# Optimization experiments

Measured on AMD Instinct MI355X. Metric: run time of the kernel, lower is better.

Reference implementation:

```python
import jax, jax.numpy as jnp
import numpy as np

B, K, D, E, V, T = 128, 49, 512, 256, 10000, 20


def setup_inputs() -> dict:
    key = jax.random.key(0)
    ks = jax.random.split(key, 20)
    rn = lambda k, shape, s=0.02: jax.random.normal(k, shape, jnp.float32) * s
    lengths = jnp.sort(jax.random.randint(ks[3], (B,), 1, T + 1))[::-1]
    lengths = lengths.at[0].set(T)  # max(lengths) == T, sorted descending
    return {
        "spatial": jax.random.normal(ks[0], (B, K, D), jnp.float32),
        "global_feats": jax.random.normal(ks[1], (B, D), jnp.float32),
        "captions": jax.random.randint(ks[2], (B, T), 0, V),
        "lengths": lengths,
        "emb": rn(ks[4], (V, E), 0.05),
        "W_init_h": rn(ks[5], (D, D)), "b_init_h": jnp.zeros((D,), jnp.float32),
        "W_init_m": rn(ks[6], (D, D)), "b_init_m": jnp.zeros((D,), jnp.float32),
        "W_ih": rn(ks[7], (4 * D, E + D)), "b_ih": jnp.zeros((4 * D,), jnp.float32),
        "W_hh": rn(ks[8], (4 * D, D)), "b_hh": jnp.zeros((4 * D,), jnp.float32),
        "Wv": rn(ks[9], (K, D)), "bv": jnp.zeros((K,), jnp.float32),
        "Wg": rn(ks[10], (K, D)), "bg": jnp.zeros((K,), jnp.float32),
        "wh": rn(ks[11], (1, K)), "bh_att": jnp.zeros((1,), jnp.float32),
        "Wp": rn(ks[12], (V, D)), "bp": jnp.zeros((V,), jnp.float32),
    }


def reference(spatial, global_feats, captions, lengths, emb,
              W_init_h, b_init_h, W_init_m, b_init_m,
              W_ih, b_ih, W_hh, b_hh,
              Wv, bv, Wg, bg, wh, bh_att, Wp, bp):
    # initialize_state
    h0 = global_feats @ W_init_h.T + b_init_h  # [B,D]
    m0 = global_feats @ W_init_m.T + b_init_m
    emb_seq = emb[captions]                     # [B,T,E]
    V_proj = spatial @ Wv.T + bv                # [B,K,K] (attn hidden = k), loop-invariant

    def step(carry, xs):
        h, m = carry
        w, t = xs                               # w: [B,E]
        active = (lengths > t)[:, None]         # masked equivalent of shrinking batch
        x = jnp.concatenate([w, global_feats], axis=1)  # [B,E+D]
        gates = x @ W_ih.T + b_ih + h @ W_hh.T + b_hh   # [B,4D]
        i, f, g, o = jnp.split(gates, 4, axis=1)        # torch LSTMCell gate order
        i, f, o = jax.nn.sigmoid(i), jax.nn.sigmoid(f), jax.nn.sigmoid(o)
        g = jnp.tanh(g)
        m_new = f * m + i * g
        h_new = o * jnp.tanh(m_new)
        h = jnp.where(active, h_new, h)
        m = jnp.where(active, m_new, m)
        # spatial attention: z = w_h^T tanh(W_v V + W_g h)
        z = jnp.tanh(V_proj + (h @ Wg.T + bg)[:, None, :]) @ wh[0] + bh_att[0]  # [B,K]
        alpha = jax.nn.softmax(z, axis=1)
        c = jnp.einsum('bk,bkd->bd', alpha, spatial)
        logit = (c + h) @ Wp.T + bp             # [B,V]
        logit = jnp.where(active, logit, 0.0)
        return (h, m), logit

    xs = (emb_seq.transpose(1, 0, 2), jnp.arange(T))
    (_, _), logits = jax.lax.scan(step, (h0, m0), xs)
    return logits.transpose(1, 0, 2)            # [B,T,V]
```

## Files before the change

kernel.cpp:

```cpp
#include <hip/hip_runtime.h>
#include <hip/hip_bf16.h>
#include <math.h>

typedef __bf16 bf16;
typedef __bf16 v8bf __attribute__((ext_vector_type(8)));
typedef __bf16 v4bfv __attribute__((ext_vector_type(4)));
typedef float  v4f  __attribute__((ext_vector_type(4)));

#define B_   128
#define KK_  49
#define D_   512
#define E_   256
#define V_   10000
#define T_   20
#define NG_  2048
#define XK_  768
#define VPAD 10112
#define NP_  128
#define NBLK 64

#define GLOAD_LDS16(gp, lp) \
    __builtin_amdgcn_global_load_lds((const __attribute__((address_space(1))) void*)(gp), \
                                     (__attribute__((address_space(3))) void*)(lp), 16, 0, 0)

__device__ inline v4bfv cvt4(float4 v) {
    v4bfv o; o[0] = (bf16)v.x; o[1] = (bf16)v.y; o[2] = (bf16)v.z; o[3] = (bf16)v.w;
    return o;
}

__global__ void prep_kernel(
    const float* __restrict__ spatial, const float* __restrict__ gfeat,
    const int* __restrict__ caps, const float* __restrict__ emb,
    const float* __restrict__ W_init_h, const float* __restrict__ b_init_h,
    const float* __restrict__ W_init_m, const float* __restrict__ b_init_m,
    const float* __restrict__ W_ih, const float* __restrict__ b_ih,
    const float* __restrict__ W_hh, const float* __restrict__ b_hh,
    const float* __restrict__ Wv, const float* __restrict__ bv,
    const float* __restrict__ Wg, const float* __restrict__ bg,
    const float* __restrict__ Wp,
    bf16* __restrict__ Wp_b, bf16* __restrict__ Whh_b, bf16* __restrict__ Wih_b,
    bf16* __restrict__ Xin_b, bf16* __restrict__ Sp_b,
    bf16* __restrict__ Wv_b, bf16* __restrict__ Wg_b,
    bf16* __restrict__ Winit2_b, bf16* __restrict__ Gf_b,
    float* __restrict__ bias_comb, float* __restrict__ bias_init,
    float* __restrict__ bv_pad, float* __restrict__ bg_pad,
    int* __restrict__ flags)
{
    const int stride = gridDim.x * blockDim.x;
    const int tid0 = blockIdx.x * blockDim.x + threadIdx.x;
    const float4 z4 = make_float4(0.f, 0.f, 0.f, 0.f);

    for (int i = tid0; i < NBLK * 32; i += stride) flags[i] = 0;

    for (int i4 = tid0; i4 < VPAD * D_ / 4; i4 += stride) {
        int row = i4 >> 7;
        float4 v = (row < V_) ? ((const float4*)Wp)[i4] : z4;
        ((v4bfv*)Wp_b)[i4] = cvt4(v);
    }
    for (int i4 = tid0; i4 < NG_ * D_ / 4; i4 += stride)
        ((v4bfv*)Whh_b)[i4] = cvt4(((const float4*)W_hh)[i4]);
    for (int i4 = tid0; i4 < NG_ * XK_ / 4; i4 += stride)
        ((v4bfv*)Wih_b)[i4] = cvt4(((const float4*)W_ih)[i4]);
    for (int i4 = tid0; i4 < T_ * B_ * XK_ / 4; i4 += stride) {
        int r = i4 / (XK_ / 4), c4 = i4 - r * (XK_ / 4);
        int c = c4 * 4;
        int t = r >> 7, b = r & 127;
        float4 v;
        if (c < E_) v = *(const float4*)&emb[(long)caps[b * T_ + t] * E_ + c];
        else        v = *(const float4*)&gfeat[(long)b * D_ + (c - E_)];
        ((v4bfv*)Xin_b)[i4] = cvt4(v);
    }
    for (int i4 = tid0; i4 < B_ * KK_ * D_ / 4; i4 += stride)
        ((v4bfv*)Sp_b)[i4] = cvt4(((const float4*)spatial)[i4]);
    for (int i4 = tid0; i4 < NP_ * D_ / 4; i4 += stride) {
        int row = i4 >> 7;
        ((v4bfv*)Wv_b)[i4] = cvt4((row < KK_) ? ((const float4*)Wv)[i4] : z4);
        ((v4bfv*)Wg_b)[i4] = cvt4((row < KK_) ? ((const float4*)Wg)[i4] : z4);
    }
    for (int i4 = tid0; i4 < 2 * D_ * D_ / 4; i4 += stride) {
        int row = i4 >> 7;
        float4 v = (row < D_) ? ((const float4*)W_init_h)[i4]
                              : ((const float4*)W_init_m)[i4 - D_ * (D_ / 4)];
        ((v4bfv*)Winit2_b)[i4] = cvt4(v);
    }
    for (int i4 = tid0; i4 < B_ * D_ / 4; i4 += stride)
        ((v4bfv*)Gf_b)[i4] = cvt4(((const float4*)gfeat)[i4]);
    for (int i = tid0; i < NG_; i += stride) bias_comb[i] = b_ih[i] + b_hh[i];
    for (int i = tid0; i < 2 * D_; i += stride)
        bias_init[i] = (i < D_) ? b_init_h[i] : b_init_m[i - D_];
    for (int i = tid0; i < NP_; i += stride) {
        bv_pad[i] = (i < KK_) ? bv[i] : 0.f;
        bg_pad[i] = (i < KK_) ? bg[i] : 0.f;
    }
}

template <int OUTMODE>
__global__ __launch_bounds__(256, 4) void gemm_bt(
    const bf16* __restrict__ A, const bf16* __restrict__ Bm,
    const float* __restrict__ bias, void* __restrict__ Cout, void* __restrict__ Cout2,
    int M, int N, int K, int out_stride, int n_real, const int* __restrict__ lengths)
{
    __shared__ bf16 As[2 * 128 * 32];
    __shared__ bf16 Bs[2 * 128 * 32];
    const int m0 = blockIdx.x * 128, n0 = blockIdx.y * 128;
    const int tid = threadIdx.x;
    const int w = tid >> 6, l = tid & 63;
    const int wm = (w >> 1) * 64, wn = (w & 1) * 64;
    const int lr = l & 15, lq = l >> 4;

    v4f acc[4][4] = {};

    for (int k0 = 0; k0 < K; k0 += 64) {
        __syncthreads();
        #pragma unroll
        for (int c = 0; c < 4; c++) {
            int u = c * 256 + tid;
            int h = u >> 9, v = u & 511;
            int row = v >> 2, kc = (v & 3) * 8;
            int u0 = c * 256 + (tid & ~63);
            GLOAD_LDS16(&A[(long)(m0 + row) * K + k0 + h * 32 + kc], &As[u0 * 8]);
            GLOAD_LDS16(&Bm[(long)(n0 + row) * K + k0 + h * 32 + kc], &Bs[u0 * 8]);
        }
        __syncthreads();
        #pragma unroll
        for (int h = 0; h < 2; h++) {
            v8bf af[4], bfv[4];
            #pragma unroll
            for (int s = 0; s < 4; s++) {
                af[s]  = *(const v8bf*)&As[h * 4096 + (wm + s * 16 + lr) * 32 + lq * 8];
                bfv[s] = *(const v8bf*)&Bs[h * 4096 + (wn + s * 16 + lr) * 32 + lq * 8];
            }
            #pragma unroll
            for (int i = 0; i < 4; i++)
                #pragma unroll
                for (int j = 0; j < 4; j++)
                    acc[i][j] = __builtin_amdgcn_mfma_f32_16x16x32_bf16(af[i], bfv[j], acc[i][j], 0, 0, 0);
        }
    }

    #pragma unroll
    for (int i = 0; i < 4; i++)
        #pragma unroll
        for (int j = 0; j < 4; j++)
            #pragma unroll
            for (int r = 0; r < 4; r++) {
                int m = m0 + wm + i * 16 + lq * 4 + r;
                int n = n0 + wn + j * 16 + lr;
                float v = acc[i][j][r];
                if (OUTMODE == 2) {
                    if (n < n_real) {
                        int t = m % T_, b = m / T_;
                        float o = (t < lengths[b]) ? (v + bias[n]) : 0.f;
                        ((float*)Cout)[(long)m * out_stride + n] = o;
                    }
                } else if (OUTMODE == 3) {
                    if (n < D_) ((bf16*)Cout)[(long)m * D_ + n] = (bf16)(v + bias[n]);
                    else ((float*)Cout2)[(long)m * D_ + n - D_] = v + bias[n];
                } else {
                    ((float*)Cout)[(long)m * out_stride + n] = v + bias[n];
                }
            }
}

__global__ __launch_bounds__(256) void lstm_persist(
    bf16* __restrict__ Hb16, const bf16* __restrict__ Whh_b,
    const float* __restrict__ Xpre, const float* __restrict__ mbuf,
    const int* __restrict__ lengths, int* __restrict__ flags)
{
    const int tid = threadIdx.x;
    const int w = tid >> 6, l = tid & 63;
    const int lr = l & 15, lq = l >> 4;
    const int bt = blockIdx.x & 1, dt = blockIdx.x >> 1;
    const int b0 = bt * 64, d0 = dt * 16;

    __shared__ bf16 Bl[64][520];

    for (int u = tid; u < 64 * 64; u += 256) {
        int row = u >> 6, kc = (u & 63) * 8;
        int g = row >> 4, dd = row & 15;
        *(v8bf*)&Bl[row][kc] = *(const v8bf*)&Whh_b[(long)(g * D_ + d0 + dd) * D_ + kc];
    }

    const int d = d0 + lr;
    float m_st[4], h_st[4];
    float xpf[4][4];
    int lenr[4];
    #pragma unroll
    for (int r = 0; r < 4; r++) {
        int b = b0 + w * 16 + lq * 4 + r;
        lenr[r] = lengths[b];
        m_st[r] = mbuf[(long)b * D_ + d];
        h_st[r] = (float)Hb16[(long)b * D_ + d];
        #pragma unroll
        for (int g = 0; g < 4; g++)
            xpf[r][g] = Xpre[(long)b * NG_ + g * D_ + d];
    }
    __syncthreads();

    for (int t = 0; t < T_; t++) {
        const bf16* Arow = Hb16 + (long)t * B_ * D_ + (long)(b0 + w * 16 + lr) * D_;
        v4f acc[4] = {};
        #pragma unroll
        for (int kk = 0; kk < 16; kk++) {
            v8bf a = *(const v8bf*)&Arow[kk * 32 + lq * 8];
            #pragma unroll
            for (int g = 0; g < 4; g++) {
                v8bf bv = *(const v8bf*)&Bl[g * 16 + lr][kk * 32 + lq * 8];
                acc[g] = __builtin_amdgcn_mfma_f32_16x16x32_bf16(a, bv, acc[g], 0, 0, 0);
            }
        }

        bf16* hn = Hb16 + (long)(t + 1) * B_ * D_;
        #pragma unroll
        for (int r = 0; r < 4; r++) {
            int b = b0 + w * 16 + lq * 4 + r;
            float gi = acc[0][r] + xpf[r][0];
            float gf = acc[1][r] + xpf[r][1];
            float gc = acc[2][r] + xpf[r][2];
            float go = acc[3][r] + xpf[r][3];
            gi = 1.f / (1.f + expf(-gi));
            gf = 1.f / (1.f + expf(-gf));
            gc = tanhf(gc);
            go = 1.f / (1.f + expf(-go));
            float m_new = gf * m_st[r] + gi * gc;
            float h_new = go * tanhf(m_new);
            bool active = t < lenr[r];
            m_st[r] = active ? m_new : m_st[r];
            h_st[r] = active ? h_new : h_st[r];
            hn[(long)b * D_ + d] = (bf16)h_st[r];
        }

        if (t + 1 < T_) {
            __syncthreads();
            if (tid == 0) {
                __threadfence();
                __hip_atomic_store(&flags[blockIdx.x * 32], t + 1,
                                   __ATOMIC_RELAXED, __HIP_MEMORY_SCOPE_AGENT);
            }
            #pragma unroll
            for (int r = 0; r < 4; r++) {
                int b = b0 + w * 16 + lq * 4 + r;
                #pragma unroll
                for (int g = 0; g < 4; g++)
                    xpf[r][g] = Xpre[(long)(t + 1) * B_ * NG_ + (long)b * NG_ + g * D_ + d];
            }
            if (w == 0) {
                int need = t + 1, v = need;
                do {
                    if (l < 32)
                        v = __hip_atomic_load(&flags[(2 * l + bt) * 32],
                                              __ATOMIC_RELAXED, __HIP_MEMORY_SCOPE_AGENT);
                } while (__any(v < need));
                __threadfence();
            }
            __syncthreads();
        }
    }
}

__global__ __launch_bounds__(256) void attn_kernel(
    const bf16* __restrict__ Hb16, const float* __restrict__ g_all,
    const float* __restrict__ Vproj, const float* __restrict__ wh,
    const bf16* __restrict__ Sp_b, bf16* __restrict__ ctx)
{
    const int w = threadIdx.x >> 6, l = threadIdx.x & 63;
    const int b = blockIdx.x / 5, tg = blockIdx.x % 5;
    const int t = tg * 4 + w;
    const int r = t * 128 + b;
    __shared__ float svp[KK_][53];
    __shared__ float sg[4][64], sal[4][64], swh[64];

    for (int p = threadIdx.x; p < KK_ * 64; p += 256) {
        int k = p >> 6, j = p & 63;
        if (j < KK_) svp[k][j] = Vproj[((long)b * KK_ + k) * NP_ + j];
    }
    if (w == 0) swh[l] = (l < KK_) ? wh[l] : 0.f;
    sg[w][l] = (l < KK_) ? g_all[(long)r * NP_ + l] : 0.f;
    __syncthreads();

    float z = -1e30f;
    if (l < KK_) {
        float a = 0.f;
        for (int j = 0; j < KK_; j++)
            a += swh[j] * tanhf(svp[l][j] + sg[w][j]);
        z = a;
    }
    float mx = z;
    #pragma unroll
    for (int o = 32; o > 0; o >>= 1) mx = fmaxf(mx, __shfl_xor(mx, o));
    float e = (l < KK_) ? expf(z - mx) : 0.f;
    float sm = e;
    #pragma unroll
    for (int o = 32; o > 0; o >>= 1) sm += __shfl_xor(sm, o);
    sal[w][l] = e / sm;
    __syncthreads();

    const bf16* hrow = Hb16 + (long)(t + 1) * B_ * D_ + (long)b * D_;
    const bf16* sp = Sp_b + (long)b * KK_ * D_;
    bf16* crow = ctx + (long)(b * T_ + t) * D_;
    v8bf hro = *(const v8bf*)&hrow[l * 8];
    float c[8] = {};
    for (int k = 0; k < KK_; k++) {
        v8bf s8 = *(const v8bf*)&sp[k * D_ + l * 8];
        float al = sal[w][k];
        #pragma unroll
        for (int e2 = 0; e2 < 8; e2++) c[e2] += al * (float)s8[e2];
    }
    v8bf outv;
    #pragma unroll
    for (int e2 = 0; e2 < 8; e2++) outv[e2] = (bf16)(c[e2] + (float)hro[e2]);
    *(v8bf*)&crow[l * 8] = outv;
}

extern "C" void kernel_launch(void* const* d_in, const int* in_sizes, int n_in,
                              void* d_out, int out_size, void* d_ws, size_t ws_size,
                              hipStream_t stream)
{
    const float* spatial  = (const float*)d_in[0];
    const float* gfeat    = (const float*)d_in[1];
    const int*   caps     = (const int*)d_in[2];
    const int*   lengths  = (const int*)d_in[3];
    const float* emb      = (const float*)d_in[4];
    const float* W_init_h = (const float*)d_in[5];
    const float* b_init_h = (const float*)d_in[6];
    const float* W_init_m = (const float*)d_in[7];
    const float* b_init_m = (const float*)d_in[8];
    const float* W_ih     = (const float*)d_in[9];
    const float* b_ih     = (const float*)d_in[10];
    const float* W_hh     = (const float*)d_in[11];
    const float* b_hh     = (const float*)d_in[12];
    const float* Wv       = (const float*)d_in[13];
    const float* bv       = (const float*)d_in[14];
    const float* Wg       = (const float*)d_in[15];
    const float* bg       = (const float*)d_in[16];
    const float* wh       = (const float*)d_in[17];
    const float* bh_att   = (const float*)d_in[18];
    const float* Wp       = (const float*)d_in[19];
    const float* bp       = (const float*)d_in[20];
    float* out = (float*)d_out;
    (void)bh_att;

    char* ws = (char*)d_ws;
    size_t off = 0;
    auto alloc = [&](size_t bytes) -> void* {
        off = (off + 255) & ~(size_t)255;
        void* p = ws + off;
        off += bytes;
        return p;
    };

    bf16* Wp_b    = (bf16*)alloc((size_t)VPAD * D_ * 2);
    bf16* Whh_b   = (bf16*)alloc((size_t)NG_ * D_ * 2);
    bf16* Wih_b   = (bf16*)alloc((size_t)NG_ * XK_ * 2);
    bf16* Xin_b   = (bf16*)alloc((size_t)T_ * B_ * XK_ * 2);
    bf16* Sp_b    = (bf16*)alloc((size_t)B_ * KK_ * D_ * 2);
    bf16* Wv_b    = (bf16*)alloc((size_t)NP_ * D_ * 2);
    bf16* Wg_b    = (bf16*)alloc((size_t)NP_ * D_ * 2);
    bf16* Winit2_b= (bf16*)alloc((size_t)2 * D_ * D_ * 2);
    bf16* Gf_b    = (bf16*)alloc((size_t)B_ * D_ * 2);
    float* bias_comb = (float*)alloc(NG_ * 4);
    float* bias_init = (float*)alloc(2 * D_ * 4);
    float* bv_pad    = (float*)alloc(NP_ * 4);
    float* bg_pad    = (float*)alloc(NP_ * 4);
    bf16* Hb16    = (bf16*)alloc((size_t)(T_ + 1) * B_ * D_ * 2);
    float* mbuf   = (float*)alloc((size_t)B_ * D_ * 4);
    float* Xpre   = (float*)alloc((size_t)T_ * B_ * NG_ * 4);
    float* VprojW = (float*)alloc((size_t)B_ * KK_ * NP_ * 4);
    float* g_allW = (float*)alloc((size_t)T_ * B_ * NP_ * 4);
    bf16* ctx     = (bf16*)alloc((size_t)T_ * B_ * D_ * 2);
    int*  flags   = (int*)alloc((size_t)NBLK * 32 * 4);

    prep_kernel<<<1024, 256, 0, stream>>>(
        spatial, gfeat, caps, emb, W_init_h, b_init_h, W_init_m, b_init_m,
        W_ih, b_ih, W_hh, b_hh, Wv, bv, Wg, bg, Wp,
        Wp_b, Whh_b, Wih_b, Xin_b, Sp_b, Wv_b, Wg_b, Winit2_b, Gf_b,
        bias_comb, bias_init, bv_pad, bg_pad, flags);

    gemm_bt<3><<<dim3(1, 8), 256, 0, stream>>>(Gf_b, Winit2_b, bias_init,
                                               Hb16, mbuf, B_, 2 * D_, D_, 0, 0, nullptr);

    gemm_bt<0><<<dim3((B_ * KK_) / 128, 1), 256, 0, stream>>>(
        Sp_b, Wv_b, bv_pad, VprojW, nullptr, B_ * KK_, NP_, D_, NP_, 0, nullptr);

    gemm_bt<0><<<dim3((T_ * B_) / 128, NG_ / 128), 256, 0, stream>>>(
        Xin_b, Wih_b, bias_comb, Xpre, nullptr, T_ * B_, NG_, XK_, NG_, 0, nullptr);

    lstm_persist<<<NBLK, 256, 0, stream>>>(Hb16, Whh_b, Xpre, mbuf, lengths, flags);

    gemm_bt<0><<<dim3((T_ * B_) / 128, 1), 256, 0, stream>>>(
        Hb16 + (size_t)B_ * D_, Wg_b, bg_pad, g_allW, nullptr, T_ * B_, NP_, D_, NP_, 0, nullptr);

    attn_kernel<<<B_ * 5, 256, 0, stream>>>(Hb16, g_allW, VprojW, wh, Sp_b, ctx);

    gemm_bt<2><<<dim3((T_ * B_) / 128, VPAD / 128), 256, 0, stream>>>(
        ctx, Wp_b, bp, out, nullptr, T_ * B_, VPAD, D_, V_, V_, lengths);
}
```

Before: 475.2 us.

## Confine persistent LSTM blocks to a single XCD with leader election

The persistent LSTM kernel now launches a larger grid. Each block reads its XCD id and takes a slot through an atomic counter. The first XCD to gather 32 blocks wins the leader election and runs the recurrence; all other blocks exit. Each surviving block computes 32 hidden columns instead of 16, the explicit threadfences are dropped, and h is written with nontemporal stores. The aim is to keep per-step flag synchronisation inside one XCD's L2 and halve the number of participating blocks, cutting inter-block barrier latency. The cost is relying on same-XCD coherence without fences, plus the extra launch and election overhead.

```diff
diff --git a/kernel.cpp b/kernel.cpp
--- a/kernel.cpp
+++ b/kernel.cpp
@@ -18,6 +18,12 @@
 #define VPAD 10112
 #define NP_  128
 #define NBLK 64
+#define LGRID 256
+
+#define FLG_CNT    1024
+#define FLG_READY  1040
+#define FLG_LEADER 1056
+#define FLG_DONE   1057
 
 #define GLOAD_LDS16(gp, lp) \
     __builtin_amdgcn_global_load_lds((const __attribute__((address_space(1))) void*)(gp), \
@@ -167,95 +173,140 @@
     const float* __restrict__ Xpre, const float* __restrict__ mbuf,
     const int* __restrict__ lengths, int* __restrict__ flags)
 {
+    __shared__ bf16 Bl[128][520];
+    __shared__ int s_info[2];
     const int tid = threadIdx.x;
+
+    if (tid == 0) {
+        int xcd;
+        asm volatile("s_getreg_b32 %0, hwreg(HW_REG_XCC_ID)" : "=s"(xcd));
+        xcd &= 15;
+        int slot = __hip_atomic_fetch_add(&flags[FLG_CNT + xcd], 1,
+                                          __ATOMIC_RELAXED, __HIP_MEMORY_SCOPE_AGENT);
+        if (slot == 31) {
+            int exp = 0;
+            bool win = __hip_atomic_compare_exchange_strong(
+                &flags[FLG_LEADER], &exp, xcd + 1,
+                __ATOMIC_RELAXED, __ATOMIC_RELAXED, __HIP_MEMORY_SCOPE_AGENT);
+            __hip_atomic_store(&flags[FLG_READY + xcd], win ? 1 : 2,
+                               __ATOMIC_RELAXED, __HIP_MEMORY_SCOPE_AGENT);
+        }
+        int st;
+        if (slot < 32) {
+            int dn;
+            do {
+                st = __hip_atomic_load(&flags[FLG_READY + xcd],
+                                       __ATOMIC_RELAXED, __HIP_MEMORY_SCOPE_AGENT);
+                dn = __hip_atomic_load(&flags[FLG_DONE],
+                                       __ATOMIC_RELAXED, __HIP_MEMORY_SCOPE_AGENT);
+            } while (st == 0 && dn == 0);
+            if (st == 0) st = 2;
+        } else st = 2;
+        s_info[0] = st;
+        s_info[1] = slot;
+    }
+    __syncthreads();
+    if (s_info[0] != 1) return;
+
+    const int slot = s_info[1];
     const int w = tid >> 6, l = tid & 63;
     const int lr = l & 15, lq = l >> 4;
-    const int bt = blockIdx.x & 1, dt = blockIdx.x >> 1;
-    const int b0 = bt * 64, d0 = dt * 16;
-
-    __shared__ bf16 Bl[64][520];
-
-    for (int u = tid; u < 64 * 64; u += 256) {
+    const int rh = slot & 1;
+    const int d0v = (slot >> 1) * 32;
+    const int b0 = rh * 64;
+
+    for (int u = tid; u < 128 * 64; u += 256) {
         int row = u >> 6, kc = (u & 63) * 8;
-        int g = row >> 4, dd = row & 15;
-        *(v8bf*)&Bl[row][kc] = *(const v8bf*)&Whh_b[(long)(g * D_ + d0 + dd) * D_ + kc];
-    }
-
-    const int d = d0 + lr;
-    float m_st[4], h_st[4];
-    float xpf[4][4];
+        int g = row >> 5, dd = row & 31;
+        *(v8bf*)&Bl[row][kc] = *(const v8bf*)&Whh_b[(long)(g * D_ + d0v + dd) * D_ + kc];
+    }
+
+    const int brow = b0 + w * 16 + lq * 4;
+    float m_st[4][2], h_st[4][2], xpf[4][2][4];
     int lenr[4];
     #pragma unroll
     for (int r = 0; r < 4; r++) {
-        int b = b0 + w * 16 + lq * 4 + r;
+        int b = brow + r;
         lenr[r] = lengths[b];
-        m_st[r] = mbuf[(long)b * D_ + d];
-        h_st[r] = (float)Hb16[(long)b * D_ + d];
-        #pragma unroll
-        for (int g = 0; g < 4; g++)
-            xpf[r][g] = Xpre[(long)b * NG_ + g * D_ + d];
+        #pragma unroll
+        for (int dh = 0; dh < 2; dh++) {
+            int d = d0v + dh * 16 + lr;
+            m_st[r][dh] = mbuf[(long)b * D_ + d];
+            h_st[r][dh] = (float)Hb16[(long)b * D_ + d];
+            #pragma unroll
+            for (int g = 0; g < 4; g++)
+                xpf[r][dh][g] = Xpre[(long)b * NG_ + g * D_ + d];
+        }
     }
     __syncthreads();
 
     for (int t = 0; t < T_; t++) {
         const bf16* Arow = Hb16 + (long)t * B_ * D_ + (long)(b0 + w * 16 + lr) * D_;
-        v4f acc[4] = {};
+        v4f acc[8] = {};
         #pragma unroll
         for (int kk = 0; kk < 16; kk++) {
             v8bf a = *(const v8bf*)&Arow[kk * 32 + lq * 8];
             #pragma unroll
-            for (int g = 0; g < 4; g++) {
-                v8bf bv = *(const v8bf*)&Bl[g * 16 + lr][kk * 32 + lq * 8];
-                acc[g] = __builtin_amdgcn_mfma_f32_16x16x32_bf16(a, bv, acc[g], 0, 0, 0);
+            for (int nt = 0; nt < 8; nt++) {
+                v8bf bv = *(const v8bf*)&Bl[nt * 16 + lr][kk * 32 + lq * 8];
+                acc[nt] = __builtin_amdgcn_mfma_f32_16x16x32_bf16(a, bv, acc[nt], 0, 0, 0);
             }
         }
 
         bf16* hn = Hb16 + (long)(t + 1) * B_ * D_;
         #pragma unroll
         for (int r = 0; r < 4; r++) {
-            int b = b0 + w * 16 + lq * 4 + r;
-            float gi = acc[0][r] + xpf[r][0];
-            float gf = acc[1][r] + xpf[r][1];
-            float gc = acc[2][r] + xpf[r][2];
-            float go = acc[3][r] + xpf[r][3];
-            gi = 1.f / (1.f + expf(-gi));
-            gf = 1.f / (1.f + expf(-gf));
-            gc = tanhf(gc);
-            go = 1.f / (1.f + expf(-go));
-            float m_new = gf * m_st[r] + gi * gc;
-            float h_new = go * tanhf(m_new);
+            int b = brow + r;
             bool active = t < lenr[r];
-            m_st[r] = active ? m_new : m_st[r];
-            h_st[r] = active ? h_new : h_st[r];
-            hn[(long)b * D_ + d] = (bf16)h_st[r];
+            #pragma unroll
+            for (int dh = 0; dh < 2; dh++) {
+                float gi = acc[0 + dh][r] + xpf[r][dh][0];
+                float gf = acc[2 + dh][r] + xpf[r][dh][1];
+                float gc = acc[4 + dh][r] + xpf[r][dh][2];
+                float go = acc[6 + dh][r] + xpf[r][dh][3];
+                gi = 1.f / (1.f + expf(-gi));
+                gf = 1.f / (1.f + expf(-gf));
+                gc = tanhf(gc);
+                go = 1.f / (1.f + expf(-go));
+                float m_new = gf * m_st[r][dh] + gi * gc;
+                float h_new = go * tanhf(m_new);
+                m_st[r][dh] = active ? m_new : m_st[r][dh];
+                h_st[r][dh] = active ? h_new : h_st[r][dh];
+                bf16 hv = (bf16)h_st[r][dh];
+                __builtin_nontemporal_store(__builtin_bit_cast(short, hv),
+                    (short*)&hn[(long)b * D_ + d0v + dh * 16 + lr]);
+            }
         }
 
         if (t + 1 < T_) {
             __syncthreads();
-            if (tid == 0) {
-                __threadfence();
-                __hip_atomic_store(&flags[blockIdx.x * 32], t + 1,
+            if (tid == 0)
+                __hip_atomic_store(&flags[slot * 32], t + 1,
                                    __ATOMIC_RELAXED, __HIP_MEMORY_SCOPE_AGENT);
-            }
             #pragma unroll
             for (int r = 0; r < 4; r++) {
-                int b = b0 + w * 16 + lq * 4 + r;
+                int b = brow + r;
                 #pragma unroll
-                for (int g = 0; g < 4; g++)
-                    xpf[r][g] = Xpre[(long)(t + 1) * B_ * NG_ + (long)b * NG_ + g * D_ + d];
+                for (int dh = 0; dh < 2; dh++)
+                    #pragma unroll
+                    for (int g = 0; g < 4; g++)
+                        xpf[r][dh][g] = Xpre[(long)(t + 1) * B_ * NG_ + (long)b * NG_
+                                             + g * D_ + d0v + dh * 16 + lr];
             }
             if (w == 0) {
                 int need = t + 1, v = need;
                 do {
-                    if (l < 32)
-                        v = __hip_atomic_load(&flags[(2 * l + bt) * 32],
+                    if (l < 16)
+                        v = __hip_atomic_load(&flags[(2 * l + rh) * 32],
                                               __ATOMIC_RELAXED, __HIP_MEMORY_SCOPE_AGENT);
                 } while (__any(v < need));
-                __threadfence();
             }
             __syncthreads();
         }
     }
+
+    if (slot == 0 && tid == 0)
+        __hip_atomic_store(&flags[FLG_DONE], 1, __ATOMIC_RELAXED, __HIP_MEMORY_SCOPE_AGENT);
 }
 
 __global__ __launch_bounds__(256) void attn_kernel(
@@ -385,7 +436,7 @@
     gemm_bt<0><<<dim3((T_ * B_) / 128, NG_ / 128), 256, 0, stream>>>(
         Xin_b, Wih_b, bias_comb, Xpre, nullptr, T_ * B_, NG_, XK_, NG_, 0, nullptr);
 
-    lstm_persist<<<NBLK, 256, 0, stream>>>(Hb16, Whh_b, Xpre, mbuf, lengths, flags);
+    lstm_persist<<<LGRID, 256, 0, stream>>>(Hb16, Whh_b, Xpre, mbuf, lengths, flags);
 
     gemm_bt<0><<<dim3((T_ * B_) / 128, 1), 256, 0, stream>>>(
         Hb16 + (size_t)B_ * D_, Wg_b, bg_pad, g_allW, nullptr, T_ * B_, NP_, D_, NP_, 0, nullptr);
```

Result: slower. 502.0 us (+5.6%).

## Replace persistent LSTM kernel with per-timestep launches and fast transcendentals

Applied to the files above, without the earlier changes.

The persistent LSTM kernel, which synchronised its blocks with global flag spin-waits, is replaced by one kernel launch per timestep that reloads its W_hh slice into LDS each time and keeps the cell state in global memory. Inactive rows copy the previous h forward instead of keeping it in registers. Sigmoid and tanh now use __expf/__fdividef approximations, both in the LSTM and in the attention kernel. This removes the spin-barrier cost but adds 20 launch overheads plus repeated weight loads, and the fast math lowers precision slightly.

```diff
diff --git a/kernel.cpp b/kernel.cpp
--- a/kernel.cpp
+++ b/kernel.cpp
@@ -26,6 +26,13 @@
 __device__ inline v4bfv cvt4(float4 v) {
     v4bfv o; o[0] = (bf16)v.x; o[1] = (bf16)v.y; o[2] = (bf16)v.z; o[3] = (bf16)v.w;
     return o;
+}
+
+__device__ inline float fsig(float x) {
+    return __fdividef(1.f, 1.f + __expf(-x));
+}
+__device__ inline float ftanh(float x) {
+    return 1.f - 2.f * __fdividef(1.f, 1.f + __expf(2.f * x));
 }
 
 __global__ void prep_kernel(
@@ -162,99 +169,75 @@
             }
 }
 
-__global__ __launch_bounds__(256) void lstm_persist(
+__global__ __launch_bounds__(256) void lstm_step(
     bf16* __restrict__ Hb16, const bf16* __restrict__ Whh_b,
-    const float* __restrict__ Xpre, const float* __restrict__ mbuf,
-    const int* __restrict__ lengths, int* __restrict__ flags)
-{
+    const float* __restrict__ Xpre, float* __restrict__ mbuf,
+    const int* __restrict__ lengths, int t)
+{
+    __shared__ bf16 Wl[64][520];
     const int tid = threadIdx.x;
+    const int bt = blockIdx.x & 1, dt = blockIdx.x >> 1;
+    const int b0 = bt * 64, d0 = dt * 16;
     const int w = tid >> 6, l = tid & 63;
     const int lr = l & 15, lq = l >> 4;
-    const int bt = blockIdx.x & 1, dt = blockIdx.x >> 1;
-    const int b0 = bt * 64, d0 = dt * 16;
-
-    __shared__ bf16 Bl[64][520];
 
     for (int u = tid; u < 64 * 64; u += 256) {
         int row = u >> 6, kc = (u & 63) * 8;
         int g = row >> 4, dd = row & 15;
-        *(v8bf*)&Bl[row][kc] = *(const v8bf*)&Whh_b[(long)(g * D_ + d0 + dd) * D_ + kc];
-    }
+        *(v8bf*)&Wl[row][kc] = *(const v8bf*)&Whh_b[(long)(g * D_ + d0 + dd) * D_ + kc];
+    }
+
+    const bf16* Arow = Hb16 + (long)t * B_ * D_ + (long)(b0 + w * 16 + lr) * D_;
+    v8bf a[16];
+    #pragma unroll
+    for (int kk = 0; kk < 16; kk++)
+        a[kk] = *(const v8bf*)&Arow[kk * 32 + lq * 8];
 
     const int d = d0 + lr;
-    float m_st[4], h_st[4];
-    float xpf[4][4];
+    const int brow = b0 + w * 16 + lq * 4;
+    float xp[4][4], m_st[4];
     int lenr[4];
     #pragma unroll
     for (int r = 0; r < 4; r++) {
-        int b = b0 + w * 16 + lq * 4 + r;
+        int b = brow + r;
         lenr[r] = lengths[b];
         m_st[r] = mbuf[(long)b * D_ + d];
-        h_st[r] = (float)Hb16[(long)b * D_ + d];
         #pragma unroll
         for (int g = 0; g < 4; g++)
-            xpf[r][g] = Xpre[(long)b * NG_ + g * D_ + d];
+            xp[r][g] = Xpre[((long)t * B_ + b) * NG_ + g * D_ + d];
     }
     __syncthreads();
 
-    for (int t = 0; t < T_; t++) {
-        const bf16* Arow = Hb16 + (long)t * B_ * D_ + (long)(b0 + w * 16 + lr) * D_;
-        v4f acc[4] = {};
-        #pragma unroll
-        for (int kk = 0; kk < 16; kk++) {
-            v8bf a = *(const v8bf*)&Arow[kk * 32 + lq * 8];
-            #pragma unroll
-            for (int g = 0; g < 4; g++) {
-                v8bf bv = *(const v8bf*)&Bl[g * 16 + lr][kk * 32 + lq * 8];
-                acc[g] = __builtin_amdgcn_mfma_f32_16x16x32_bf16(a, bv, acc[g], 0, 0, 0);
-            }
+    v4f acc[4] = {};
+    #pragma unroll
+    for (int kk = 0; kk < 16; kk++) {
+        #pragma unroll
+        for (int g = 0; g < 4; g++) {
+            v8bf bv = *(const v8bf*)&Wl[g * 16 + lr][kk * 32 + lq * 8];
+            acc[g] = __builtin_amdgcn_mfma_f32_16x16x32_bf16(a[kk], bv, acc[g], 0, 0, 0);
         }
-
-        bf16* hn = Hb16 + (long)(t + 1) * B_ * D_;
-        #pragma unroll
-        for (int r = 0; r < 4; r++) {
-            int b = b0 + w * 16 + lq * 4 + r;
-            float gi = acc[0][r] + xpf[r][0];
-            float gf = acc[1][r] + xpf[r][1];
-            float gc = acc[2][r] + xpf[r][2];
-            float go = acc[3][r] + xpf[r][3];
-            gi = 1.f / (1.f + expf(-gi));
-            gf = 1.f / (1.f + expf(-gf));
-            gc = tanhf(gc);
-            go = 1.f / (1.f + expf(-go));
-            float m_new = gf * m_st[r] + gi * gc;
-            float h_new = go * tanhf(m_new);
-            bool active = t < lenr[r];
-            m_st[r] = active ? m_new : m_st[r];
-            h_st[r] = active ? h_new : h_st[r];
-            hn[(long)b * D_ + d] = (bf16)h_st[r];
+    }
+
+    bf16* hn = Hb16 + (long)(t + 1) * B_ * D_;
+    const bf16* hp = Hb16 + (long)t * B_ * D_;
+    #pragma unroll
+    for (int r = 0; r < 4; r++) {
+        int b = brow + r;
+        bool active = t < lenr[r];
+        float gi = fsig (acc[0][r] + xp[r][0]);
+        float gf = fsig (acc[1][r] + xp[r][1]);
+        float gc = ftanh(acc[2][r] + xp[r][2]);
+        float go = fsig (acc[3][r] + xp[r][3]);
+        float m_new = gf * m_st[r] + gi * gc;
+        float h_new = go * ftanh(m_new);
+        bf16 hv;
+        if (active) {
+            mbuf[(long)b * D_ + d] = m_new;
+            hv = (bf16)h_new;
+        } else {
+            hv = hp[(long)b * D_ + d];
         }
-
-        if (t + 1 < T_) {
-            __syncthreads();
-            if (tid == 0) {
-                __threadfence();
-                __hip_atomic_store(&flags[blockIdx.x * 32], t + 1,
-                                   __ATOMIC_RELAXED, __HIP_MEMORY_SCOPE_AGENT);
-            }
-            #pragma unroll
-            for (int r = 0; r < 4; r++) {
-                int b = b0 + w * 16 + lq * 4 + r;
-                #pragma unroll
-                for (int g = 0; g < 4; g++)
-                    xpf[r][g] = Xpre[(long)(t + 1) * B_ * NG_ + (long)b * NG_ + g * D_ + d];
-            }
-            if (w == 0) {
-                int need = t + 1, v = need;
-                do {
-                    if (l < 32)
-                        v = __hip_atomic_load(&flags[(2 * l + bt) * 32],
-                                              __ATOMIC_RELAXED, __HIP_MEMORY_SCOPE_AGENT);
-                } while (__any(v < need));
-                __threadfence();
-            }
-            __syncthreads();
-        }
+        hn[(long)b * D_ + d] = hv;
     }
 }
 
@@ -282,13 +265,13 @@
     if (l < KK_) {
         float a = 0.f;
         for (int j = 0; j < KK_; j++)
-            a += swh[j] * tanhf(svp[l][j] + sg[w][j]);
+            a += swh[j] * ftanh(svp[l][j] + sg[w][j]);
         z = a;
     }
     float mx = z;
     #pragma unroll
     for (int o = 32; o > 0; o >>= 1) mx = fmaxf(mx, __shfl_xor(mx, o));
-    float e = (l < KK_) ? expf(z - mx) : 0.f;
+    float e = (l < KK_) ? __expf(z - mx) : 0.f;
     float sm = e;
     #pragma unroll
     for (int o = 32; o > 0; o >>= 1) sm += __shfl_xor(sm, o);
@@ -385,7 +368,8 @@
     gemm_bt<0><<<dim3((T_ * B_) / 128, NG_ / 128), 256, 0, stream>>>(
         Xin_b, Wih_b, bias_comb, Xpre, nullptr, T_ * B_, NG_, XK_, NG_, 0, nullptr);
 
-    lstm_persist<<<NBLK, 256, 0, stream>>>(Hb16, Whh_b, Xpre, mbuf, lengths, flags);
+    for (int t = 0; t < T_; ++t)
+        lstm_step<<<64, 256, 0, stream>>>(Hb16, Whh_b, Xpre, mbuf, lengths, t);
 
     gemm_bt<0><<<dim3((T_ * B_) / 128, 1), 256, 0, stream>>>(
         Hb16 + (size_t)B_ * D_, Wg_b, bg_pad, g_allW, nullptr, T_ * B_, NP_, D_, NP_, 0, nullptr);
```

Result: no change. 479.7 us (+1.0%).
